# Performance work log

Hardware: AMD Instinct MI355X
Metric: run time of the kernel (lower is better)

Reference implementation:

```python
import jax, jax.numpy as jnp
import numpy as np
from jax import lax

N = 2_097_152  # grid length
WENO5_MULT_BIAS = 0.1


def _conv1d(x, w, b, pad):
    # x: [1, C_in, L], w: [C_out, C_in, K] -> [1, C_out, L]
    y = lax.conv_general_dilated(x, w, window_strides=(1,), padding=[(pad, pad)],
                                 dimension_numbers=('NCH', 'OIH', 'NCH'))
    return y + b[None, :, None]


def _inner_nn_weno5(dif, w1, b1, w2, b2, w3, b3, w4, b4, w5, b5, w6, b6):
    # dif: [N] -> multiplier signal [N] in (0,1) via sigmoid
    x = dif[None, None, :]
    x = jax.nn.elu(_conv1d(x, w1, b1, 2))
    x = jax.nn.elu(_conv1d(x, w2, b2, 2))
    x = jax.nn.elu(_conv1d(x, w3, b3, 0))
    x = jax.nn.elu(_conv1d(x, w4, b4, 0))
    x = jax.nn.elu(_conv1d(x, w5, b5, 1))
    x = jax.nn.sigmoid(_conv1d(x, w6, b6, 0))
    return x[0, 0, :]


def _avg_diff(uu):
    # centered average of forward differences, replicated at the edges -> [N]
    dif = uu[1:] - uu[:-1]
    dif_left = jnp.concatenate([dif, dif[-1:]])
    dif_right = jnp.concatenate([dif[:1], dif])
    return 0.5 * dif_left + 0.5 * dif_right


def _fluxes_minus(u):
    f0 = (11 * u[3:-2] - 7 * u[4:-1] + 2 * u[5:]) / 6
    f1 = (2 * u[2:-3] + 5 * u[3:-2] - u[4:-1]) / 6
    f2 = (-u[1:-4] + 5 * u[2:-3] + 2 * u[3:-2]) / 6
    return f0, f1, f2


def _betas_minus(u):
    b0 = 13 / 12 * (u[3:-2] - 2 * u[4:-1] + u[5:]) ** 2 + 1 / 4 * (3 * u[3:-2] - 4 * u[4:-1] + u[5:]) ** 2
    b1 = 13 / 12 * (u[2:-3] - 2 * u[3:-2] + u[4:-1]) ** 2 + 1 / 4 * (u[2:-3] - u[4:-1]) ** 2
    b2 = 13 / 12 * (u[1:-4] - 2 * u[2:-3] + u[3:-2]) ** 2 + 1 / 4 * (u[1:-4] - 4 * u[2:-3] + 3 * u[3:-2]) ** 2
    return b0, b1, b2


def _weno5(uu, e, beta_mult):
    # w5_minus=True, mweno=True, mapped=False, trainable=True branch
    ur = uu[1:]
    ul = uu[:-1]
    fp = _fluxes_minus(ur)
    fn = _fluxes_minus(ul)
    bp = _betas_minus(ur)
    bn = _betas_minus(ul)
    # multipliers bm[3+shift:-3+shift] for shift in {-1,0,1}
    mul = (beta_mult[2:-4], beta_mult[3:-3], beta_mult[4:-2])
    bp = [b * m for b, m in zip(bp, mul)]
    bn = [b * m for b, m in zip(bn, mul)]
    ds = (1 / 10, 6 / 10, 3 / 10)

    def omegas_mweno(bs):
        brs = (bs[2] - bs[0]) ** 2
        o = [d / (e + b) ** 2 * (brs + (e + b) ** 2) for b, d in zip(bs, ds)]
        s = o[0] + o[1] + o[2]
        return [x / s for x in o]

    op = omegas_mweno(bp)
    on = omegas_mweno(bn)
    fluxp = op[0] * fp[0] + op[1] * fp[1] + op[2] * fp[2]
    fluxn = on[0] * fn[0] + on[1] * fn[1] + on[2] * fn[2]
    return fluxp - fluxn  # [N-6]


def setup_inputs() -> dict:
    key = jax.random.key(0)
    ks = jax.random.split(key, 14)
    uu = jax.random.normal(ks[0], (N,), dtype=jnp.float32)
    e = jnp.float32(1e-6)
    s = 0.1  # weight scale for stability
    w1 = s * jax.random.normal(ks[1], (20, 1, 5), jnp.float32)
    b1 = s * jax.random.normal(ks[2], (20,), jnp.float32)
    w2 = s * jax.random.normal(ks[3], (40, 20, 5), jnp.float32)
    b2 = s * jax.random.normal(ks[4], (40,), jnp.float32)
    w3 = s * jax.random.normal(ks[5], (80, 40, 1), jnp.float32)
    b3 = s * jax.random.normal(ks[6], (80,), jnp.float32)
    w4 = s * jax.random.normal(ks[7], (40, 80, 1), jnp.float32)
    b4 = s * jax.random.normal(ks[8], (40,), jnp.float32)
    w5 = s * jax.random.normal(ks[9], (20, 40, 3), jnp.float32)
    b5 = s * jax.random.normal(ks[10], (20,), jnp.float32)
    w6 = s * jax.random.normal(ks[11], (1, 20, 1), jnp.float32)
    b6 = s * jax.random.normal(ks[12], (1,), jnp.float32)
    return {"uu": uu, "e": e, "w1": w1, "b1": b1, "w2": w2, "b2": b2,
            "w3": w3, "b3": b3, "w4": w4, "b4": b4, "w5": w5, "b5": b5,
            "w6": w6, "b6": b6}


def reference(uu, e, w1, b1, w2, b2, w3, b3, w4, b4, w5, b5, w6, b6):
    dif = _avg_diff(uu)
    beta_mult = _inner_nn_weno5(dif, w1, b1, w2, b2, w3, b3, w4, b4, w5, b5, w6, b6) + WENO5_MULT_BIAS
    return _weno5(uu, e, beta_mult)
```

## Files before the change

kernel.cpp:

```cpp
#include <hip/hip_runtime.h>
#include <math.h>

#define NTHREADS 256
#define TOUT 126
#define NP 128
#define X1ROWS 132
#define X1S 40
#define NDIF 136
#define NDIFP 152
#define NUU 138

#define F2_BASE 0
#define F3_BASE 15
#define F4_BASE 25
#define F5_BASE 34
#define F1_BASE 42
#define NFRAGS 44

typedef unsigned short u16;
typedef unsigned int u32;
typedef __attribute__((ext_vector_type(8))) short bf16x8;
typedef __attribute__((ext_vector_type(4))) float f32x4;

__device__ __forceinline__ float elu_f(float x) {
    return fmaxf(x, __expf(fminf(x, 0.0f)) - 1.0f);
}
__device__ __forceinline__ float rcp_f(float x) {
    return __builtin_amdgcn_rcpf(x);
}
__device__ __forceinline__ float sq_f(float x) { return x * x; }
__device__ __forceinline__ u16 f2bf(float f) {
    union { float f; u32 u; } v; v.f = f;
    u32 r = v.u + 0x7FFFu + ((v.u >> 16) & 1u);
    return (u16)(r >> 16);
}
__device__ __forceinline__ float bf2f(u16 h) {
    union { u32 u; float f; } v; v.u = ((u32)h) << 16;
    return v.f;
}
__device__ __forceinline__ u32 pack_trunc(float a, float b) {
    union { float f; u32 u; } va, vb; va.f = a; vb.f = b;
#if __has_builtin(__builtin_amdgcn_perm)
    return __builtin_amdgcn_perm(vb.u, va.u, 0x07060302u);
#else
    return (vb.u & 0xFFFF0000u) | (va.u >> 16);
#endif
}
__device__ __forceinline__ u32 pack_rne(float a, float b) {
    return (u32)f2bf(a) | ((u32)f2bf(b) << 16);
}

__global__ __launch_bounds__(64) void build_frags_kernel(
    const float* __restrict__ w1, const float* __restrict__ w2,
    const float* __restrict__ w3, const float* __restrict__ w4,
    const float* __restrict__ w5, u16* __restrict__ ws)
{
    const int f = blockIdx.x;
    const int lane = threadIdx.x;
    const int m = lane & 15;
    const int q = lane >> 4;
    float wvv[8];
    #pragma unroll
    for (int j = 0; j < 8; ++j) wvv[j] = 0.0f;

    if (f < F3_BASE) {
        int mt = (f - F2_BASE) / 5, s = (f - F2_BASE) % 5;
        int oc = mt * 16 + m;
        #pragma unroll
        for (int j = 0; j < 8; ++j) {
            int ic = q * 8 + j;
            if (oc < 40 && ic < 20) wvv[j] = w2[oc * 100 + ic * 5 + s];
        }
    } else if (f < F4_BASE) {
        int mt = (f - F3_BASE) / 2, s = (f - F3_BASE) % 2;
        int oc = mt * 16 + m;
        #pragma unroll
        for (int j = 0; j < 8; ++j) {
            int k = s * 32 + q * 8 + j;
            if (k < 40) wvv[j] = w3[oc * 40 + k];
        }
    } else if (f < F5_BASE) {
        int mt = (f - F4_BASE) / 3, s = (f - F4_BASE) % 3;
        int oc = mt * 16 + m;
        #pragma unroll
        for (int j = 0; j < 8; ++j) {
            int k = s * 32 + q * 8 + j;
            if (oc < 40 && k < 80) wvv[j] = w4[oc * 80 + k];
        }
    } else if (f < F1_BASE) {
        int mt = (f - F5_BASE) / 4, s = (f - F5_BASE) % 4;
        int oc = mt * 16 + m;
        int k0 = s * 32 + q * 8;
        int dk = k0 / 40, ic0 = k0 - dk * 40;
        #pragma unroll
        for (int j = 0; j < 8; ++j) {
            if (oc < 20 && k0 < 120) wvv[j] = w5[oc * 120 + (ic0 + j) * 3 + dk];
        }
    } else {
        int mt = f - F1_BASE;
        int oc = mt * 16 + m;
        #pragma unroll
        for (int j = 0; j < 8; ++j) {
            int k = q * 8 + j;
            if (oc < 20 && k < 5) wvv[j] = w1[oc * 5 + k];
        }
    }
    u32 pk[4];
    #pragma unroll
    for (int p = 0; p < 4; ++p)
        pk[p] = (u32)f2bf(wvv[2 * p]) | ((u32)f2bf(wvv[2 * p + 1]) << 16);
    u32* wp = (u32*)&ws[(f * 64 + lane) * 8];
    wp[0] = pk[0]; wp[1] = pk[1]; wp[2] = pk[2]; wp[3] = pk[3];
}

__device__ __forceinline__ bf16x8 ld_frag(const u16* ws, int f, int lane) {
    return *(const bf16x8*)&ws[(f * 64 + lane) * 8];
}

__global__ __launch_bounds__(NTHREADS, 2) void weno_nn_kernel(
    const float* __restrict__ uu, const float* __restrict__ e_ptr,
    const float* __restrict__ w1, const float* __restrict__ b1,
    const float* __restrict__ b2, const float* __restrict__ b3,
    const float* __restrict__ b4, const float* __restrict__ b5,
    const float* __restrict__ w6, const float* __restrict__ b6,
    const u16* __restrict__ wfr,
    float* __restrict__ out, int n_out, int N)
{
    __shared__ float s_uu[NUU];
    __shared__ float s_dif[NDIFP];
    __shared__ __align__(16) u16 bufA[2 * NP * 40];
    __shared__ __align__(16) u16 bufB[130 * 40];

    float* s_beta = s_dif;

    const int tid  = threadIdx.x;
    const int lane = tid & 63;
    const int wv_id = __builtin_amdgcn_readfirstlane(tid >> 6);
    const int m    = lane & 15;
    const int q    = lane >> 4;
    const int J0   = blockIdx.x * TOUT;
    const int P0   = J0 + 2;
    const int U0   = J0 - 4;

    u16* t3a = bufA;
    u16* t3b = bufA + NP * 40;

    for (int i = tid; i < NUU; i += NTHREADS) {
        int g = U0 + i;
        s_uu[i] = (g >= 0 && g < N) ? uu[g] : 0.0f;
    }
    __syncthreads();

    for (int d = tid; d < NDIFP; d += NTHREADS) {
        int g = P0 - 5 + d;
        float v = 0.0f;
        if (d < NDIF && g >= 0 && g < N) {
            int j1 = g < N - 2 ? g : N - 2;
            int j0 = g - 1 > 0 ? g - 1 : 0;
            float dl = s_uu[j1 + 1 - U0] - s_uu[j1 - U0];
            float dr = s_uu[j0 + 1 - U0] - s_uu[j0 - U0];
            v = 0.5f * (dl + dr);
        }
        s_dif[d] = v;
    }
    __syncthreads();

    {
        bf16x8 a1[2];
        a1[0] = ld_frag(wfr, F1_BASE + 0, lane);
        a1[1] = ld_frag(wfr, F1_BASE + 1, lane);
        f32x4 bias1[2];
        #pragma unroll
        for (int r = 0; r < 4; ++r) {
            bias1[0][r] = b1[4 * q + r];
            int oc = 16 + 4 * q + r;
            bias1[1][r] = (oc < 20) ? b1[oc] : 0.0f;
        }
        for (int idx = wv_id; idx < 9; idx += 4) {
            const int N0 = idx * 16;
            float d0 = s_dif[N0 + m + 0];
            float d1 = s_dif[N0 + m + 1];
            float d2 = s_dif[N0 + m + 2];
            float d3 = s_dif[N0 + m + 3];
            float d4 = s_dif[N0 + m + 4];
            bf16x8 bfrag;
            u32* bw = (u32*)&bfrag;
            bw[0] = pack_rne(d0, d1);
            bw[1] = pack_rne(d2, d3);
            bw[2] = pack_rne(d4, 0.0f);
            bw[3] = 0;
            f32x4 acc0 = bias1[0];
            f32x4 acc1 = bias1[1];
            acc0 = __builtin_amdgcn_mfma_f32_16x16x32_bf16(a1[0], bfrag, acc0, 0, 0, 0);
            acc1 = __builtin_amdgcn_mfma_f32_16x16x32_bf16(a1[1], bfrag, acc1, 0, 0, 0);
            int pos = N0 + m;
            if (pos < X1ROWS) {
                int g = P0 - 3 + pos;
                bool valid = (g >= 0 && g < N);
                float e0 = valid ? elu_f(acc0[0]) : 0.0f;
                float e1 = valid ? elu_f(acc0[1]) : 0.0f;
                float e2 = valid ? elu_f(acc0[2]) : 0.0f;
                float e3 = valid ? elu_f(acc0[3]) : 0.0f;
                u32* wp = (u32*)&bufA[pos * X1S + 4 * q];
                wp[0] = pack_trunc(e0, e1);
                wp[1] = pack_trunc(e2, e3);
                if (q == 0) {
                    float f0 = valid ? elu_f(acc1[0]) : 0.0f;
                    float f1 = valid ? elu_f(acc1[1]) : 0.0f;
                    float f2 = valid ? elu_f(acc1[2]) : 0.0f;
                    float f3 = valid ? elu_f(acc1[3]) : 0.0f;
                    u32* wp2 = (u32*)&bufA[pos * X1S + 16];
                    wp2[0] = pack_trunc(f0, f1);
                    wp2[1] = pack_trunc(f2, f3);
                } else {
                    u32* wpz = (u32*)&bufA[pos * X1S + 20 + (q - 1) * 4];
                    wpz[0] = 0; wpz[1] = 0;
                }
            }
        }
    }
    __syncthreads();

    {
        bf16x8 a2[3][5];
        #pragma unroll
        for (int mt = 0; mt < 3; ++mt)
            #pragma unroll
            for (int s = 0; s < 5; ++s)
                a2[mt][s] = ld_frag(wfr, F2_BASE + mt * 5 + s, lane);
        f32x4 bias2[3];
        #pragma unroll
        for (int mt = 0; mt < 3; ++mt) {
            #pragma unroll
            for (int r = 0; r < 4; ++r) {
                int oc = mt * 16 + 4 * q + r;
                bias2[mt][r] = (oc < 40) ? b2[oc] : 0.0f;
            }
        }
        for (int t = 0; t < 2; ++t) {
            const int N0 = (wv_id * 2 + t) * 16;
            f32x4 acc[3];
            #pragma unroll
            for (int mt = 0; mt < 3; ++mt) acc[mt] = bias2[mt];
            #pragma unroll
            for (int s = 0; s < 5; ++s) {
                bf16x8 bfrag = *(const bf16x8*)&bufA[(N0 + m + s) * X1S + q * 8];
                #pragma unroll
                for (int mt = 0; mt < 3; ++mt)
                    acc[mt] = __builtin_amdgcn_mfma_f32_16x16x32_bf16(a2[mt][s], bfrag, acc[mt], 0, 0, 0);
            }
            #pragma unroll
            for (int mt = 0; mt < 3; ++mt) {
                int oc0 = mt * 16 + 4 * q;
                if (oc0 < 40) {
                    u32* wp = (u32*)&bufB[(N0 + m) * 40 + oc0];
                    wp[0] = pack_trunc(elu_f(acc[mt][0]), elu_f(acc[mt][1]));
                    wp[1] = pack_trunc(elu_f(acc[mt][2]), elu_f(acc[mt][3]));
                }
            }
        }
    }
    __syncthreads();

    {
        bf16x8 a3[5][2];
        #pragma unroll
        for (int mt = 0; mt < 5; ++mt)
            #pragma unroll
            for (int s = 0; s < 2; ++s)
                a3[mt][s] = ld_frag(wfr, F3_BASE + mt * 2 + s, lane);
        f32x4 bias3[5];
        #pragma unroll
        for (int mt = 0; mt < 5; ++mt) {
            #pragma unroll
            for (int r = 0; r < 4; ++r) bias3[mt][r] = b3[mt * 16 + 4 * q + r];
        }
        for (int t = 0; t < 2; ++t) {
            const int N0 = (wv_id * 2 + t) * 16;
            f32x4 acc[5];
            #pragma unroll
            for (int mt = 0; mt < 5; ++mt) acc[mt] = bias3[mt];
            {
                bf16x8 bfrag = *(const bf16x8*)&bufB[(N0 + m) * 40 + q * 8];
                #pragma unroll
                for (int mt = 0; mt < 5; ++mt)
                    acc[mt] = __builtin_amdgcn_mfma_f32_16x16x32_bf16(a3[mt][0], bfrag, acc[mt], 0, 0, 0);
            }
            {
                bf16x8 bfrag = *(const bf16x8*)&bufB[(N0 + m) * 40 + ((q == 0) ? 32 : 0)];
                #pragma unroll
                for (int mt = 0; mt < 5; ++mt)
                    acc[mt] = __builtin_amdgcn_mfma_f32_16x16x32_bf16(a3[mt][1], bfrag, acc[mt], 0, 0, 0);
            }
            const int row = N0 + m;
            #pragma unroll
            for (int mt = 0; mt < 5; ++mt) {
                int oc0 = mt * 16 + 4 * q;
                u16* dst;
                if (mt < 2)       dst = &t3a[row * 40 + oc0];
                else if (mt >= 3) dst = &t3b[row * 40 + (oc0 - 40)];
                else              dst = (oc0 < 40) ? &t3a[row * 40 + oc0]
                                                   : &t3b[row * 40 + (oc0 - 40)];
                u32* wp = (u32*)dst;
                wp[0] = pack_trunc(elu_f(acc[mt][0]), elu_f(acc[mt][1]));
                wp[1] = pack_trunc(elu_f(acc[mt][2]), elu_f(acc[mt][3]));
            }
        }
    }
    __syncthreads();

    {
        bf16x8 a4[3][3];
        #pragma unroll
        for (int mt = 0; mt < 3; ++mt)
            #pragma unroll
            for (int s = 0; s < 3; ++s)
                a4[mt][s] = ld_frag(wfr, F4_BASE + mt * 3 + s, lane);
        f32x4 bias4[3];
        #pragma unroll
        for (int mt = 0; mt < 3; ++mt) {
            #pragma unroll
            for (int r = 0; r < 4; ++r) {
                int oc = mt * 16 + 4 * q + r;
                bias4[mt][r] = (oc < 40) ? b4[oc] : 0.0f;
            }
        }
        if (tid < 80) bufB[128 * 40 + tid] = 0;
        for (int t = 0; t < 2; ++t) {
            const int N0 = (wv_id * 2 + t) * 16;
            const int row = N0 + m;
            f32x4 acc[3];
            #pragma unroll
            for (int mt = 0; mt < 3; ++mt) acc[mt] = bias4[mt];
            #pragma unroll
            for (int s = 0; s < 3; ++s) {
                int k0 = s * 32 + q * 8;
                const u16* src;
                if (s == 0)       src = &t3a[row * 40 + k0];
                else if (s == 1)  src = (q == 0) ? &t3a[row * 40 + 32]
                                                 : &t3b[row * 40 + (k0 - 40)];
                else              src = (q < 2)  ? &t3b[row * 40 + (k0 - 40)]
                                                 : &t3a[row * 40];
                bf16x8 bfrag = *(const bf16x8*)src;
                #pragma unroll
                for (int mt = 0; mt < 3; ++mt)
                    acc[mt] = __builtin_amdgcn_mfma_f32_16x16x32_bf16(a4[mt][s], bfrag, acc[mt], 0, 0, 0);
            }
            #pragma unroll
            for (int mt = 0; mt < 3; ++mt) {
                int oc0 = mt * 16 + 4 * q;
                if (oc0 < 40) {
                    u32* wp = (u32*)&bufB[row * 40 + oc0];
                    wp[0] = pack_trunc(elu_f(acc[mt][0]), elu_f(acc[mt][1]));
                    wp[1] = pack_trunc(elu_f(acc[mt][2]), elu_f(acc[mt][3]));
                }
            }
        }
    }
    __syncthreads();

    {
        bf16x8 a5[2][4];
        #pragma unroll
        for (int mt = 0; mt < 2; ++mt)
            #pragma unroll
            for (int s = 0; s < 4; ++s)
                a5[mt][s] = ld_frag(wfr, F5_BASE + mt * 4 + s, lane);
        f32x4 bias5[2];
        #pragma unroll
        for (int mt = 0; mt < 2; ++mt) {
            #pragma unroll
            for (int r = 0; r < 4; ++r) {
                int oc = mt * 16 + 4 * q + r;
                bias5[mt][r] = (oc < 20) ? b5[oc] : 0.0f;
            }
        }
        float w6a[4], w6b[4];
        #pragma unroll
        for (int r = 0; r < 4; ++r) {
            w6a[r] = w6[4 * q + r];
            w6b[r] = (q == 0) ? w6[16 + r] : 0.0f;
        }
        const float b6v = b6[0];

        for (int t = 0; t < 2; ++t) {
            const int N0 = (wv_id * 2 + t) * 16;
            f32x4 acc[2];
            #pragma unroll
            for (int mt = 0; mt < 2; ++mt) acc[mt] = bias5[mt];
            #pragma unroll
            for (int s = 0; s < 4; ++s) {
                int k0 = s * 32 + q * 8;
                int dk = (k0 < 120) ? (k0 / 40) : 0;
                int ic0 = (k0 < 120) ? (k0 - dk * 40) : 0;
                bf16x8 bfrag = *(const bf16x8*)&bufB[(N0 + m + dk) * 40 + ic0];
                #pragma unroll
                for (int mt = 0; mt < 2; ++mt)
                    acc[mt] = __builtin_amdgcn_mfma_f32_16x16x32_bf16(a5[mt][s], bfrag, acc[mt], 0, 0, 0);
            }
            float p = 0.0f;
            #pragma unroll
            for (int r = 0; r < 4; ++r) p += w6a[r] * elu_f(acc[0][r]);
            #pragma unroll
            for (int r = 0; r < 4; ++r) p += w6b[r] * elu_f(acc[1][r]);
            p += __shfl_xor(p, 16);
            p += __shfl_xor(p, 32);
            float aa = p + b6v;
            if (q == 0)
                s_beta[N0 + m] = rcp_f(1.0f + __expf(-aa)) + 0.1f;
        }
    }
    __syncthreads();

    const float eps = e_ptr[0];
    if (tid < TOUT) {
        int j = J0 + tid;
        if (j < n_out) {
            float a  = s_uu[tid + 5];
            float b  = s_uu[tid + 6];
            float c  = s_uu[tid + 7];
            float d  = s_uu[tid + 8];
            float ee = s_uu[tid + 9];
            float f  = s_uu[tid + 10];
            float m0 = s_beta[tid];
            float m1 = s_beta[tid + 1];
            float m2 = s_beta[tid + 2];

            const float i6 = 1.0f / 6.0f;
            float fp0 = (11.f * d - 7.f * ee + 2.f * f) * i6;
            float fp1 = (2.f * c + 5.f * d - ee) * i6;
            float fp2 = (-b + 5.f * c + 2.f * d) * i6;
            float fn0 = (11.f * c - 7.f * d + 2.f * ee) * i6;
            float fn1 = (2.f * b + 5.f * c - d) * i6;
            float fn2 = (-a + 5.f * b + 2.f * c) * i6;

            const float c1312 = 13.f / 12.f;
            float bp0 = c1312 * sq_f(d - 2.f * ee + f) + 0.25f * sq_f(3.f * d - 4.f * ee + f);
            float bp1 = c1312 * sq_f(c - 2.f * d + ee) + 0.25f * sq_f(c - ee);
            float bp2 = c1312 * sq_f(b - 2.f * c + d) + 0.25f * sq_f(b - 4.f * c + 3.f * d);
            float bn0 = c1312 * sq_f(c - 2.f * d + ee) + 0.25f * sq_f(3.f * c - 4.f * d + ee);
            float bn1 = c1312 * sq_f(b - 2.f * c + d) + 0.25f * sq_f(b - d);
            float bn2 = c1312 * sq_f(a - 2.f * b + c) + 0.25f * sq_f(a - 4.f * b + 3.f * c);

            bp0 *= m0; bp1 *= m1; bp2 *= m2;
            bn0 *= m0; bn1 *= m1; bn2 *= m2;

            float q0 = eps + bp0; q0 *= q0;
            float q1 = eps + bp1; q1 *= q1;
            float q2 = eps + bp2; q2 *= q2;
            float brs = bp2 - bp0; brs *= brs;
            float o0 = 0.1f * (1.f + brs * rcp_f(q0));
            float o1 = 0.6f * (1.f + brs * rcp_f(q1));
            float o2 = 0.3f * (1.f + brs * rcp_f(q2));
            float inv = rcp_f(o0 + o1 + o2);
            float fluxp = (o0 * fp0 + o1 * fp1 + o2 * fp2) * inv;

            q0 = eps + bn0; q0 *= q0;
            q1 = eps + bn1; q1 *= q1;
            q2 = eps + bn2; q2 *= q2;
            brs = bn2 - bn0; brs *= brs;
            o0 = 0.1f * (1.f + brs * rcp_f(q0));
            o1 = 0.6f * (1.f + brs * rcp_f(q1));
            o2 = 0.3f * (1.f + brs * rcp_f(q2));
            inv = rcp_f(o0 + o1 + o2);
            float fluxn = (o0 * fn0 + o1 * fn1 + o2 * fn2) * inv;

            out[j] = fluxp - fluxn;
        }
    }
}

extern "C" void kernel_launch(void* const* d_in, const int* in_sizes, int n_in,
                              void* d_out, int out_size, void* d_ws, size_t ws_size,
                              hipStream_t stream) {
    const float* uu = (const float*)d_in[0];
    const float* e  = (const float*)d_in[1];
    const float* w1 = (const float*)d_in[2];
    const float* b1 = (const float*)d_in[3];
    const float* w2 = (const float*)d_in[4];
    const float* b2 = (const float*)d_in[5];
    const float* w3 = (const float*)d_in[6];
    const float* b3 = (const float*)d_in[7];
    const float* w4 = (const float*)d_in[8];
    const float* b4 = (const float*)d_in[9];
    const float* w5 = (const float*)d_in[10];
    const float* b5 = (const float*)d_in[11];
    const float* w6 = (const float*)d_in[12];
    const float* b6 = (const float*)d_in[13];
    float* out = (float*)d_out;
    u16* wfr = (u16*)d_ws;
    const int N = in_sizes[0];
    const int nblocks = (out_size + TOUT - 1) / TOUT;

    build_frags_kernel<<<NFRAGS, 64, 0, stream>>>(w1, w2, w3, w4, w5, wfr);
    weno_nn_kernel<<<nblocks, NTHREADS, 0, stream>>>(
        uu, e, w1, b1, b2, b3, b4, b5, w6, b6, wfr,
        out, out_size, N);
}
```

Measured before the change: 267.9 us.

## Use per-wave private buffers with halo recompute to drop block barriers

Each wave now computes its own layer-1 rows, including a 4-row halo, into a private LDS region. Layers 2 and 3 then read only data produced by the same wave, so three block-wide barriers become compiler scheduling barriers. The final 20-to-1 projection moves from an in-register shuffle reduction to a bf16 LDS staging step plus a per-thread scalar dot product. That adds one block barrier and rounds layer-5 activations to bf16 before the projection. Layer 1 is partly recomputed for the halo, and the LDS footprint grows.

```diff
diff --git a/kernel.cpp b/kernel.cpp
--- a/kernel.cpp
+++ b/kernel.cpp
@@ -4,11 +4,13 @@
 #define NTHREADS 256
 #define TOUT 126
 #define NP 128
-#define X1ROWS 132
 #define X1S 40
+#define T3S 88
+#define X5S 26
 #define NDIF 136
 #define NDIFP 152
 #define NUU 138
+#define WREG 2816
 
 #define F2_BASE 0
 #define F3_BASE 15
@@ -128,7 +130,7 @@
 {
     __shared__ float s_uu[NUU];
     __shared__ float s_dif[NDIFP];
-    __shared__ __align__(16) u16 bufA[2 * NP * 40];
+    __shared__ __align__(16) u16 bufA[4 * WREG];
     __shared__ __align__(16) u16 bufB[130 * 40];
 
     float* s_beta = s_dif;
@@ -142,8 +144,7 @@
     const int P0   = J0 + 2;
     const int U0   = J0 - 4;
 
-    u16* t3a = bufA;
-    u16* t3b = bufA + NP * 40;
+    u16* xw = &bufA[wv_id * WREG];
 
     for (int i = tid; i < NUU; i += NTHREADS) {
         int g = U0 + i;
@@ -165,6 +166,7 @@
     }
     __syncthreads();
 
+
     {
         bf16x8 a1[2];
         a1[0] = ld_frag(wfr, F1_BASE + 0, lane);
@@ -176,13 +178,15 @@
             int oc = 16 + 4 * q + r;
             bias1[1][r] = (oc < 20) ? b1[oc] : 0.0f;
         }
-        for (int idx = wv_id; idx < 9; idx += 4) {
-            const int N0 = idx * 16;
-            float d0 = s_dif[N0 + m + 0];
-            float d1 = s_dif[N0 + m + 1];
-            float d2 = s_dif[N0 + m + 2];
-            float d3 = s_dif[N0 + m + 3];
-            float d4 = s_dif[N0 + m + 4];
+        #pragma unroll
+        for (int it = 0; it < 3; ++it) {
+            const int li = it * 16 + m;
+            const int pos = wv_id * 32 + li;
+            float d0 = s_dif[pos + 0];
+            float d1 = s_dif[pos + 1];
+            float d2 = s_dif[pos + 2];
+            float d3 = s_dif[pos + 3];
+            float d4 = s_dif[pos + 4];
             bf16x8 bfrag;
             u32* bw = (u32*)&bfrag;
             bw[0] = pack_rne(d0, d1);
@@ -193,15 +197,14 @@
             f32x4 acc1 = bias1[1];
             acc0 = __builtin_amdgcn_mfma_f32_16x16x32_bf16(a1[0], bfrag, acc0, 0, 0, 0);
             acc1 = __builtin_amdgcn_mfma_f32_16x16x32_bf16(a1[1], bfrag, acc1, 0, 0, 0);
-            int pos = N0 + m;
-            if (pos < X1ROWS) {
+            if (li < 36) {
                 int g = P0 - 3 + pos;
                 bool valid = (g >= 0 && g < N);
                 float e0 = valid ? elu_f(acc0[0]) : 0.0f;
                 float e1 = valid ? elu_f(acc0[1]) : 0.0f;
                 float e2 = valid ? elu_f(acc0[2]) : 0.0f;
                 float e3 = valid ? elu_f(acc0[3]) : 0.0f;
-                u32* wp = (u32*)&bufA[pos * X1S + 4 * q];
+                u32* wp = (u32*)&xw[li * X1S + 4 * q];
                 wp[0] = pack_trunc(e0, e1);
                 wp[1] = pack_trunc(e2, e3);
                 if (q == 0) {
@@ -209,17 +212,17 @@
                     float f1 = valid ? elu_f(acc1[1]) : 0.0f;
                     float f2 = valid ? elu_f(acc1[2]) : 0.0f;
                     float f3 = valid ? elu_f(acc1[3]) : 0.0f;
-                    u32* wp2 = (u32*)&bufA[pos * X1S + 16];
+                    u32* wp2 = (u32*)&xw[li * X1S + 16];
                     wp2[0] = pack_trunc(f0, f1);
                     wp2[1] = pack_trunc(f2, f3);
                 } else {
-                    u32* wpz = (u32*)&bufA[pos * X1S + 20 + (q - 1) * 4];
+                    u32* wpz = (u32*)&xw[li * X1S + 20 + (q - 1) * 4];
                     wpz[0] = 0; wpz[1] = 0;
                 }
             }
         }
     }
-    __syncthreads();
+    __builtin_amdgcn_sched_barrier(0);
 
     {
         bf16x8 a2[3][5];
@@ -238,13 +241,14 @@
             }
         }
         for (int t = 0; t < 2; ++t) {
-            const int N0 = (wv_id * 2 + t) * 16;
+            const int lr = t * 16 + m;
+            const int gr = wv_id * 32 + lr;
             f32x4 acc[3];
             #pragma unroll
             for (int mt = 0; mt < 3; ++mt) acc[mt] = bias2[mt];
             #pragma unroll
             for (int s = 0; s < 5; ++s) {
-                bf16x8 bfrag = *(const bf16x8*)&bufA[(N0 + m + s) * X1S + q * 8];
+                bf16x8 bfrag = *(const bf16x8*)&xw[(lr + s) * X1S + q * 8];
                 #pragma unroll
                 for (int mt = 0; mt < 3; ++mt)
                     acc[mt] = __builtin_amdgcn_mfma_f32_16x16x32_bf16(a2[mt][s], bfrag, acc[mt], 0, 0, 0);
@@ -253,14 +257,14 @@
             for (int mt = 0; mt < 3; ++mt) {
                 int oc0 = mt * 16 + 4 * q;
                 if (oc0 < 40) {
-                    u32* wp = (u32*)&bufB[(N0 + m) * 40 + oc0];
+                    u32* wp = (u32*)&bufB[gr * 40 + oc0];
                     wp[0] = pack_trunc(elu_f(acc[mt][0]), elu_f(acc[mt][1]));
                     wp[1] = pack_trunc(elu_f(acc[mt][2]), elu_f(acc[mt][3]));
                 }
             }
         }
     }
-    __syncthreads();
+    __builtin_amdgcn_sched_barrier(0);
 
     {
         bf16x8 a3[5][2];
@@ -276,38 +280,33 @@
             for (int r = 0; r < 4; ++r) bias3[mt][r] = b3[mt * 16 + 4 * q + r];
         }
         for (int t = 0; t < 2; ++t) {
-            const int N0 = (wv_id * 2 + t) * 16;
+            const int lr = t * 16 + m;
+            const int gr = wv_id * 32 + lr;
             f32x4 acc[5];
             #pragma unroll
             for (int mt = 0; mt < 5; ++mt) acc[mt] = bias3[mt];
             {
-                bf16x8 bfrag = *(const bf16x8*)&bufB[(N0 + m) * 40 + q * 8];
+                bf16x8 bfrag = *(const bf16x8*)&bufB[gr * 40 + q * 8];
                 #pragma unroll
                 for (int mt = 0; mt < 5; ++mt)
                     acc[mt] = __builtin_amdgcn_mfma_f32_16x16x32_bf16(a3[mt][0], bfrag, acc[mt], 0, 0, 0);
             }
             {
-                bf16x8 bfrag = *(const bf16x8*)&bufB[(N0 + m) * 40 + ((q == 0) ? 32 : 0)];
+                bf16x8 bfrag = *(const bf16x8*)&bufB[gr * 40 + ((q == 0) ? 32 : 0)];
                 #pragma unroll
                 for (int mt = 0; mt < 5; ++mt)
                     acc[mt] = __builtin_amdgcn_mfma_f32_16x16x32_bf16(a3[mt][1], bfrag, acc[mt], 0, 0, 0);
             }
-            const int row = N0 + m;
             #pragma unroll
             for (int mt = 0; mt < 5; ++mt) {
                 int oc0 = mt * 16 + 4 * q;
-                u16* dst;
-                if (mt < 2)       dst = &t3a[row * 40 + oc0];
-                else if (mt >= 3) dst = &t3b[row * 40 + (oc0 - 40)];
-                else              dst = (oc0 < 40) ? &t3a[row * 40 + oc0]
-                                                   : &t3b[row * 40 + (oc0 - 40)];
-                u32* wp = (u32*)dst;
+                u32* wp = (u32*)&xw[lr * T3S + oc0];
                 wp[0] = pack_trunc(elu_f(acc[mt][0]), elu_f(acc[mt][1]));
                 wp[1] = pack_trunc(elu_f(acc[mt][2]), elu_f(acc[mt][3]));
             }
         }
     }
-    __syncthreads();
+    __builtin_amdgcn_sched_barrier(0);
 
     {
         bf16x8 a4[3][3];
@@ -327,21 +326,15 @@
         }
         if (tid < 80) bufB[128 * 40 + tid] = 0;
         for (int t = 0; t < 2; ++t) {
-            const int N0 = (wv_id * 2 + t) * 16;
-            const int row = N0 + m;
+            const int lr = t * 16 + m;
+            const int gr = wv_id * 32 + lr;
             f32x4 acc[3];
             #pragma unroll
             for (int mt = 0; mt < 3; ++mt) acc[mt] = bias4[mt];
             #pragma unroll
             for (int s = 0; s < 3; ++s) {
                 int k0 = s * 32 + q * 8;
-                const u16* src;
-                if (s == 0)       src = &t3a[row * 40 + k0];
-                else if (s == 1)  src = (q == 0) ? &t3a[row * 40 + 32]
-                                                 : &t3b[row * 40 + (k0 - 40)];
-                else              src = (q < 2)  ? &t3b[row * 40 + (k0 - 40)]
-                                                 : &t3a[row * 40];
-                bf16x8 bfrag = *(const bf16x8*)src;
+                bf16x8 bfrag = *(const bf16x8*)&xw[lr * T3S + ((k0 < 80) ? k0 : 0)];
                 #pragma unroll
                 for (int mt = 0; mt < 3; ++mt)
                     acc[mt] = __builtin_amdgcn_mfma_f32_16x16x32_bf16(a4[mt][s], bfrag, acc[mt], 0, 0, 0);
@@ -350,7 +343,7 @@
             for (int mt = 0; mt < 3; ++mt) {
                 int oc0 = mt * 16 + 4 * q;
                 if (oc0 < 40) {
-                    u32* wp = (u32*)&bufB[row * 40 + oc0];
+                    u32* wp = (u32*)&bufB[gr * 40 + oc0];
                     wp[0] = pack_trunc(elu_f(acc[mt][0]), elu_f(acc[mt][1]));
                     wp[1] = pack_trunc(elu_f(acc[mt][2]), elu_f(acc[mt][3]));
                 }
@@ -375,14 +368,6 @@
                 bias5[mt][r] = (oc < 20) ? b5[oc] : 0.0f;
             }
         }
-        float w6a[4], w6b[4];
-        #pragma unroll
-        for (int r = 0; r < 4; ++r) {
-            w6a[r] = w6[4 * q + r];
-            w6b[r] = (q == 0) ? w6[16 + r] : 0.0f;
-        }
-        const float b6v = b6[0];
-
         for (int t = 0; t < 2; ++t) {
             const int N0 = (wv_id * 2 + t) * 16;
             f32x4 acc[2];
@@ -398,17 +383,25 @@
                 for (int mt = 0; mt < 2; ++mt)
                     acc[mt] = __builtin_amdgcn_mfma_f32_16x16x32_bf16(a5[mt][s], bfrag, acc[mt], 0, 0, 0);
             }
-            float p = 0.0f;
-            #pragma unroll
-            for (int r = 0; r < 4; ++r) p += w6a[r] * elu_f(acc[0][r]);
-            #pragma unroll
-            for (int r = 0; r < 4; ++r) p += w6b[r] * elu_f(acc[1][r]);
-            p += __shfl_xor(p, 16);
-            p += __shfl_xor(p, 32);
-            float aa = p + b6v;
-            if (q == 0)
-                s_beta[N0 + m] = rcp_f(1.0f + __expf(-aa)) + 0.1f;
-        }
+            #pragma unroll
+            for (int mt = 0; mt < 2; ++mt) {
+                int oc0 = mt * 16 + 4 * q;
+                if (oc0 < 20) {
+                    u32* wp = (u32*)&bufA[(N0 + m) * X5S + oc0];
+                    wp[0] = pack_trunc(elu_f(acc[mt][0]), elu_f(acc[mt][1]));
+                    wp[1] = pack_trunc(elu_f(acc[mt][2]), elu_f(acc[mt][3]));
+                }
+            }
+        }
+    }
+    __syncthreads();
+
+    if (tid < NP) {
+        float a = b6[0];
+        #pragma unroll
+        for (int c = 0; c < 20; ++c)
+            a += w6[c] * bf2f(bufA[tid * X5S + c]);
+        s_beta[tid] = rcp_f(1.0f + __expf(-a)) + 0.1f;
     }
     __syncthreads();
 
```

After: 257.9 us, median of 3. 3.7% less time.
